# Optimization experiments

Measured on AMD Instinct MI355X. Metric: run time of the kernel, lower is better.

## Reference

```python
import jax, jax.numpy as jnp
import numpy as np

V = 33279   # num_tokens
E = 256     # embedding_size
H = 512     # hidden_size
NH = 8      # num_heads
L = 4       # num_layers
DH = E // NH
MAXPOS = 64


def _ln(x, g, b):
    mu = jnp.mean(x, axis=-1, keepdims=True)
    var = jnp.mean((x - mu) ** 2, axis=-1, keepdims=True)
    return (x - mu) / jnp.sqrt(var + 1e-5) * g + b


def setup_inputs() -> dict:
    key = jax.random.key(0)
    ks = jax.random.split(key, 32)
    N, S = 128, 64
    label = jax.random.randint(ks[0], (N, S), 0, V)
    # Bernoulli(0.15) BERT-style mask (deterministic stand-in for torch sampling)
    mask = (jax.random.uniform(ks[1], (N, S)) < 0.15).astype(jnp.int32)
    s = 0.02
    inp = {
        'label': label, 'mask': mask,
        'emb': jax.random.normal(ks[2], (V + 1, E)) * s,
        'pos': jax.random.normal(ks[3], (MAXPOS, E)) * s,
        'emb_g': jnp.ones((E,)), 'emb_b': jnp.zeros((E,)),
        # stacked per-layer params (leading dim L)
        'Wq': jax.random.normal(ks[4], (L, E, E)) * s, 'bq': jnp.zeros((L, E)),
        'Wk': jax.random.normal(ks[5], (L, E, E)) * s, 'bk': jnp.zeros((L, E)),
        'Wv': jax.random.normal(ks[6], (L, E, E)) * s, 'bv': jnp.zeros((L, E)),
        'Wo': jax.random.normal(ks[7], (L, E, E)) * s, 'bo': jnp.zeros((L, E)),
        'n1g': jnp.ones((L, E)), 'n1b': jnp.zeros((L, E)),
        'W1': jax.random.normal(ks[8], (L, E, H)) * s, 'b1': jnp.zeros((L, H)),
        'W2': jax.random.normal(ks[9], (L, H, E)) * s, 'b2': jnp.zeros((L, E)),
        'n2g': jnp.ones((L, E)), 'n2b': jnp.zeros((L, E)),
        # decoder head
        'dW1': jax.random.normal(ks[10], (E, E)) * s, 'db1': jnp.zeros((E,)),
        'dng': jnp.ones((E,)), 'dnb': jnp.zeros((E,)),
        'dW2': jax.random.normal(ks[11], (E, V)) * s, 'db2': jnp.zeros((V,)),
    }
    return inp


def reference(label, mask, emb, pos, emb_g, emb_b, Wq, bq, Wk, bk, Wv, bv,
              Wo, bo, n1g, n1b, W1, b1, W2, b2, n2g, n2b,
              dW1, db1, dng, dnb, dW2, db2):
    N, S = label.shape
    src_ids = jnp.where(mask == 1, V, label)  # masked-token id = num_tokens
    # embedding + positional, then LayerNorm (eval: Scaler/Dropout identity)
    x = emb[src_ids] + pos[:S][None, :, :]
    x = _ln(x, emb_g, emb_b)
    temp = jnp.asarray((E // NH) ** 0.5, x.dtype)

    def layer(x, p):
        wq, bq_, wk, bk_, wv, bv_, wo, bo_, g1, b1n, w1, b1_, w2, b2_, g2, b2n = p
        q = (x @ wq + bq_).reshape(N, S, NH, DH).transpose(0, 2, 1, 3)
        k = (x @ wk + bk_).reshape(N, S, NH, DH).transpose(0, 2, 1, 3)
        v = (x @ wv + bv_).reshape(N, S, NH, DH).transpose(0, 2, 1, 3)
        scores = jnp.einsum('nhsd,nhtd->nhst', q, k) / temp
        attn = jax.nn.softmax(scores, axis=-1)
        o = jnp.einsum('nhst,nhtd->nhsd', attn, v)
        o = o.transpose(0, 2, 1, 3).reshape(N, S, E) @ wo + bo_
        x1 = _ln(x + o, g1, b1n)
        ff = jax.nn.gelu(x1 @ w1 + b1_, approximate=False) @ w2 + b2_
        x2 = _ln(x1 + ff, g2, b2n)
        return x2, None

    x, _ = jax.lax.scan(layer, x, (Wq, bq, Wk, bk, Wv, bv, Wo, bo,
                                   n1g, n1b, W1, b1, W2, b2, n2g, n2b))
    # decoder head: linear -> gelu -> LN -> vocab projection
    h = jax.nn.gelu(x @ dW1 + db1, approximate=False)
    h = _ln(h, dng, dnb)
    logits = h @ dW2 + db2               # [N, S, V]
    logp = jax.nn.log_softmax(logits, axis=-1)
    loss = -jnp.take_along_axis(logp, label[..., None], axis=-1).mean()
    score = logits.transpose(0, 2, 1)    # [N, V, S] like torch permute(0,2,1)
    return score, loss
```

## Files before the change

### kernel.cpp

```cpp
#include <hip/hip_runtime.h>
#include <hip/hip_bf16.h>

#define DEVFN static __device__ __forceinline__

constexpr int N_ = 128, S_ = 64, T_ = N_ * S_;
constexpr int E_ = 256, H_ = 512, NH_ = 8, DH_ = 32, L_ = 4;
constexpr int V_ = 33279, VPAD_ = 33280, NVT_ = VPAD_ / 256;

typedef __attribute__((ext_vector_type(8))) short bf16x8;
typedef __attribute__((ext_vector_type(4))) float f32x4;
typedef unsigned short ushort_t;

DEVFN ushort_t f2bf(float f) {
  unsigned int u = __float_as_uint(f);
  unsigned int r = (u + 0x7fffu + ((u >> 16) & 1u)) >> 16;
  return (ushort_t)r;
}
DEVFN float bf2f(ushort_t u) { return __uint_as_float(((unsigned)u) << 16); }

DEVFN float geluf(float x) {
  return 0.5f * x * (1.f + erff(x * 0.70710678118654752440f));
}

DEVFN float wave_sum(float v) {
  #pragma unroll
  for (int off = 32; off >= 1; off >>= 1) v += __shfl_xor(v, off, 64);
  return v;
}

__global__ __launch_bounds__(256) void k_embed_ln(
    const int* __restrict__ label, const int* __restrict__ mask,
    const float* __restrict__ emb, const float* __restrict__ pos,
    const float* __restrict__ g, const float* __restrict__ b,
    float* __restrict__ x, ushort_t* __restrict__ xb) {
  int wv = threadIdx.x >> 6, lane = threadIdx.x & 63;
  int t = blockIdx.x * 4 + wv;
  int s = t & (S_ - 1);
  int id = (mask[t] == 1) ? V_ : label[t];
  int c = lane * 4;
  float4 v = *(const float4*)&emb[(size_t)id * E_ + c];
  float4 p = *(const float4*)&pos[s * E_ + c];
  v.x += p.x; v.y += p.y; v.z += p.z; v.w += p.w;
  float mean = wave_sum(v.x + v.y + v.z + v.w) * (1.f / E_);
  float4 d = {v.x - mean, v.y - mean, v.z - mean, v.w - mean};
  float var = wave_sum(d.x * d.x + d.y * d.y + d.z * d.z + d.w * d.w) * (1.f / E_);
  float rstd = 1.f / sqrtf(var + 1e-5f);
  float4 g4 = *(const float4*)&g[c];
  float4 b4 = *(const float4*)&b[c];
  float4 y = {d.x * rstd * g4.x + b4.x, d.y * rstd * g4.y + b4.y,
              d.z * rstd * g4.z + b4.z, d.w * rstd * g4.w + b4.w};
  *(float4*)&x[(size_t)t * E_ + c] = y;
  ushort4 yb = {f2bf(y.x), f2bf(y.y), f2bf(y.z), f2bf(y.w)};
  *(ushort4*)&xb[(size_t)t * E_ + c] = yb;
}

__global__ __launch_bounds__(256) void k_add_ln(
    const float* __restrict__ a, const float* __restrict__ bsrc,
    const float* __restrict__ g, const float* __restrict__ bet,
    float* __restrict__ y, ushort_t* __restrict__ yb) {
  int wv = threadIdx.x >> 6, lane = threadIdx.x & 63;
  int t = blockIdx.x * 4 + wv;
  int c = lane * 4;
  float4 v = *(const float4*)&a[(size_t)t * E_ + c];
  if (bsrc) {
    float4 u = *(const float4*)&bsrc[(size_t)t * E_ + c];
    v.x += u.x; v.y += u.y; v.z += u.z; v.w += u.w;
  }
  float mean = wave_sum(v.x + v.y + v.z + v.w) * (1.f / E_);
  float4 d = {v.x - mean, v.y - mean, v.z - mean, v.w - mean};
  float var = wave_sum(d.x * d.x + d.y * d.y + d.z * d.z + d.w * d.w) * (1.f / E_);
  float rstd = 1.f / sqrtf(var + 1e-5f);
  float4 g4 = *(const float4*)&g[c];
  float4 b4 = *(const float4*)&bet[c];
  float4 o = {d.x * rstd * g4.x + b4.x, d.y * rstd * g4.y + b4.y,
              d.z * rstd * g4.z + b4.z, d.w * rstd * g4.w + b4.w};
  if (y) *(float4*)&y[(size_t)t * E_ + c] = o;
  if (yb) {
    ushort4 ob = {f2bf(o.x), f2bf(o.y), f2bf(o.z), f2bf(o.w)};
    *(ushort4*)&yb[(size_t)t * E_ + c] = ob;
  }
}

__global__ __launch_bounds__(256) void k_bcat(
    const float* __restrict__ bq, const float* __restrict__ bk,
    const float* __restrict__ bv, float* __restrict__ bqkv) {
  int l = blockIdx.x, i = threadIdx.x;
  bqkv[l * 768 + i]       = bq[l * 256 + i];
  bqkv[l * 768 + 256 + i] = bk[l * 256 + i];
  bqkv[l * 768 + 512 + i] = bv[l * 256 + i];
}

__global__ __launch_bounds__(256) void k_wt(const float* __restrict__ src,
                                            ushort_t* __restrict__ dst,
                                            int K, int J, int dstLayerStride) {
  __shared__ float tile[32][33];
  int j0 = blockIdx.x * 32, k0 = blockIdx.y * 32, l = blockIdx.z;
  src += (size_t)l * K * J;
  dst += (size_t)l * dstLayerStride;
  int tx = threadIdx.x & 31, ty = threadIdx.x >> 5;
  #pragma unroll
  for (int rr = 0; rr < 4; rr++) {
    int kk = ty * 4 + rr;
    tile[kk][tx] = src[(size_t)(k0 + kk) * J + j0 + tx];
  }
  __syncthreads();
  #pragma unroll
  for (int rr = 0; rr < 4; rr++) {
    int jj = ty * 4 + rr;
    dst[(size_t)(j0 + jj) * K + k0 + tx] = f2bf(tile[tx][jj]);
  }
}

__global__ __launch_bounds__(256) void k_wtE(
    const float* __restrict__ Wq, const float* __restrict__ Wk,
    const float* __restrict__ Wv, const float* __restrict__ Wo,
    const float* __restrict__ dW1, ushort_t* __restrict__ wqkvT,
    ushort_t* __restrict__ woT, ushort_t* __restrict__ dw1T) {
  __shared__ float tile[32][33];
  int z = blockIdx.z;
  const float* src;
  ushort_t* dst;
  if (z == 4 * L_) {
    src = dW1; dst = dw1T;
  } else {
    int w = z >> 2, l = z & 3;
    const float* ws = (w == 0) ? Wq : (w == 1) ? Wk : (w == 2) ? Wv : Wo;
    src = ws + (size_t)l * E_ * E_;
    dst = (w < 3) ? (wqkvT + (size_t)l * 768 * E_ + (size_t)w * 256 * E_)
                  : (woT + (size_t)l * E_ * E_);
  }
  int j0 = blockIdx.x * 32, k0 = blockIdx.y * 32;
  int tx = threadIdx.x & 31, ty = threadIdx.x >> 5;
  #pragma unroll
  for (int rr = 0; rr < 4; rr++) {
    int kk = ty * 4 + rr;
    tile[kk][tx] = src[(size_t)(k0 + kk) * E_ + j0 + tx];
  }
  __syncthreads();
  #pragma unroll
  for (int rr = 0; rr < 4; rr++) {
    int jj = ty * 4 + rr;
    dst[(size_t)(j0 + jj) * E_ + k0 + tx] = f2bf(tile[tx][jj]);
  }
}

template <int K, int OUT_BF16, int GELU_>
__global__ __launch_bounds__(256) void k_mm(
    const ushort_t* __restrict__ Xb, const ushort_t* __restrict__ WT,
    const float* __restrict__ bias, void* __restrict__ C, int Nout) {
  constexpr int STR = K + 8;
  __shared__ ushort_t xs[64 * STR];
  int tid = threadIdx.x, lane = tid & 63, wv = tid >> 6;
  int t0 = blockIdx.x * 64, j0 = blockIdx.y * 64;
  const ushort_t* xsrc = Xb + (size_t)t0 * K;
  for (int i = tid; i < 64 * (K / 8); i += 256) {
    int r = i / (K / 8), c = (i % (K / 8)) * 8;
    *(uint4*)&xs[r * STR + c] = *(const uint4*)&xsrc[(size_t)r * K + c];
  }
  __syncthreads();
  int l15 = lane & 15, l4 = lane >> 4;
  f32x4 acc[4] = {};
  const ushort_t* xrow = &xs[(wv * 16 + l15) * STR + l4 * 8];
  const ushort_t* wrow = WT + (size_t)j0 * K + l4 * 8;
  #pragma unroll
  for (int kb = 0; kb < K / 32; kb++) {
    bf16x8 a = *(const bf16x8*)(xrow + kb * 32);
    #pragma unroll
    for (int st = 0; st < 4; st++) {
      bf16x8 bfr = *(const bf16x8*)(wrow + (size_t)(st * 16 + l15) * K + kb * 32);
      acc[st] = __builtin_amdgcn_mfma_f32_16x16x32_bf16(a, bfr, acc[st], 0, 0, 0);
    }
  }
  #pragma unroll
  for (int st = 0; st < 4; st++) {
    int j = j0 + st * 16 + l15;
    float bv_ = bias[j];
    #pragma unroll
    for (int r = 0; r < 4; r++) {
      float val = acc[st][r] + bv_;
      if (GELU_) val = geluf(val);
      int t = t0 + wv * 16 + l4 * 4 + r;
      if (OUT_BF16)
        ((ushort_t*)C)[(size_t)t * Nout + j] = f2bf(val);
      else
        ((float*)C)[(size_t)t * Nout + j] = val;
    }
  }
}

__global__ __launch_bounds__(256) void k_attn(
    const ushort_t* __restrict__ qkv, ushort_t* __restrict__ o) {
  __shared__ __align__(16) ushort_t vt_[32 * 72];
  __shared__ __align__(16) ushort_t ps[64 * 72];
  int n = blockIdx.x >> 3, h = blockIdx.x & 7;
  int tid = threadIdx.x, lane = tid & 63, wv = tid >> 6;
  int l15 = lane & 15, l4 = lane >> 4;
  const ushort_t* qbase = qkv + (size_t)n * S_ * 768 + h * DH_;
  for (int i = tid; i < S_ * DH_; i += 256) {
    int t = i >> 5, d = i & 31;
    vt_[d * 72 + t] = qbase[(size_t)t * 768 + 512 + d];
  }
  int srow = wv * 16 + l15;
  bf16x8 aq = *(const bf16x8*)&qbase[(size_t)srow * 768 + l4 * 8];
  f32x4 sc[4];
  #pragma unroll
  for (int st = 0; st < 4; st++) {
    bf16x8 bk_ = *(const bf16x8*)&qbase[(size_t)(st * 16 + l15) * 768 + 256 + l4 * 8];
    f32x4 z = {};
    sc[st] = __builtin_amdgcn_mfma_f32_16x16x32_bf16(aq, bk_, z, 0, 0, 0);
  }
  const float scale = 0.17677669529663687f;
  #pragma unroll
  for (int st = 0; st < 4; st++)
    #pragma unroll
    for (int r = 0; r < 4; r++) sc[st][r] *= scale;
  #pragma unroll
  for (int r = 0; r < 4; r++) {
    float m = fmaxf(fmaxf(sc[0][r], sc[1][r]), fmaxf(sc[2][r], sc[3][r]));
    m = fmaxf(m, __shfl_xor(m, 1, 64));
    m = fmaxf(m, __shfl_xor(m, 2, 64));
    m = fmaxf(m, __shfl_xor(m, 4, 64));
    m = fmaxf(m, __shfl_xor(m, 8, 64));
    float p0 = __expf(sc[0][r] - m), p1 = __expf(sc[1][r] - m);
    float p2 = __expf(sc[2][r] - m), p3 = __expf(sc[3][r] - m);
    float sum = p0 + p1 + p2 + p3;
    sum += __shfl_xor(sum, 1, 64);
    sum += __shfl_xor(sum, 2, 64);
    sum += __shfl_xor(sum, 4, 64);
    sum += __shfl_xor(sum, 8, 64);
    float inv = 1.f / sum;
    int prow = (wv * 16 + l4 * 4 + r) * 72;
    ps[prow + 0 * 16 + l15] = f2bf(p0 * inv);
    ps[prow + 1 * 16 + l15] = f2bf(p1 * inv);
    ps[prow + 2 * 16 + l15] = f2bf(p2 * inv);
    ps[prow + 3 * 16 + l15] = f2bf(p3 * inv);
  }
  __syncthreads();
  f32x4 oc[2] = {};
  #pragma unroll
  for (int kb = 0; kb < 2; kb++) {
    bf16x8 ap = *(const bf16x8*)&ps[srow * 72 + kb * 32 + l4 * 8];
    #pragma unroll
    for (int st2 = 0; st2 < 2; st2++) {
      bf16x8 bv_ = *(const bf16x8*)&vt_[(st2 * 16 + l15) * 72 + kb * 32 + l4 * 8];
      oc[st2] = __builtin_amdgcn_mfma_f32_16x16x32_bf16(ap, bv_, oc[st2], 0, 0, 0);
    }
  }
  ushort_t* ob = o + (size_t)n * S_ * E_ + h * DH_;
  #pragma unroll
  for (int st2 = 0; st2 < 2; st2++)
    #pragma unroll
    for (int r = 0; r < 4; r++)
      ob[(size_t)(wv * 16 + l4 * 4 + r) * E_ + st2 * 16 + l15] = f2bf(oc[st2][r]);
}

__global__ __launch_bounds__(256) void k_w2t(const float* __restrict__ w,
                                             ushort_t* __restrict__ wt) {
  __shared__ float tile[32 * 33];
  int tx = threadIdx.x & 31, ty = threadIdx.x >> 5;
  int v0 = blockIdx.x * 32, k0 = blockIdx.y * 32;
  #pragma unroll
  for (int rr = 0; rr < 4; rr++) {
    int kk = ty * 4 + rr;
    int vv = v0 + tx;
    tile[kk * 33 + tx] = (vv < V_) ? w[(size_t)(k0 + kk) * V_ + vv] : 0.f;
  }
  __syncthreads();
  #pragma unroll
  for (int rr = 0; rr < 4; rr++) {
    int vv = ty * 4 + rr;
    wt[(size_t)(v0 + vv) * E_ + k0 + tx] = f2bf(tile[tx * 33 + vv]);
  }
}

__global__ __launch_bounds__(256) void k_vocab(
    const ushort_t* __restrict__ hbf, const ushort_t* __restrict__ wt,
    const float* __restrict__ db2, float* __restrict__ out,
    float* __restrict__ pmax, float* __restrict__ psum) {
  __shared__ ushort_t hs[64 * 264];
  __shared__ float redm[4][64];
  __shared__ float reds[4][64];
  int n = blockIdx.x, vt = blockIdx.y;
  int tid = threadIdx.x, lane = tid & 63, wv = tid >> 6;
  const ushort_t* hsrc = hbf + (size_t)n * S_ * E_;
  for (int i = tid; i < (S_ * E_) / 8; i += 256) {
    int s = i >> 5, kc = (i & 31) * 8;
    *(uint4*)&hs[s * 264 + kc] = *(const uint4*)&hsrc[s * E_ + kc];
  }
  __syncthreads();
  int l15 = lane & 15, l4 = lane >> 4;
  float rm[4], rs[4];
  #pragma unroll
  for (int st = 0; st < 4; st++) { rm[st] = -INFINITY; rs[st] = 0.f; }
  #pragma unroll
  for (int h2 = 0; h2 < 2; h2++) {
    const ushort_t* Ap0 =
        wt + (size_t)(vt * 256 + h2 * 128 + wv * 16 + l15) * E_ + l4 * 8;
    const ushort_t* Ap1 = Ap0 + (size_t)64 * E_;
    f32x4 acc[2][4] = {};
    #pragma unroll
    for (int kb = 0; kb < 8; kb++) {
      bf16x8 a0 = *(const bf16x8*)(Ap0 + kb * 32);
      bf16x8 a1 = *(const bf16x8*)(Ap1 + kb * 32);
      #pragma unroll
      for (int st = 0; st < 4; st++) {
        bf16x8 bfr = *(const bf16x8*)&hs[(st * 16 + l15) * 264 + kb * 32 + l4 * 8];
        acc[0][st] = __builtin_amdgcn_mfma_f32_16x16x32_bf16(a0, bfr, acc[0][st], 0, 0, 0);
        acc[1][st] = __builtin_amdgcn_mfma_f32_16x16x32_bf16(a1, bfr, acc[1][st], 0, 0, 0);
      }
    }
    float vals[2][4][4];
    #pragma unroll
    for (int mt = 0; mt < 2; mt++) {
      #pragma unroll
      for (int j = 0; j < 4; j++) {
        int v = vt * 256 + h2 * 128 + wv * 16 + mt * 64 + l4 * 4 + j;
        bool valid = v < V_;
        float bias = valid ? db2[v] : 0.f;
        size_t ob = ((size_t)n * V_ + v) * S_;
        #pragma unroll
        for (int st = 0; st < 4; st++) {
          float val = valid ? (acc[mt][st][j] + bias) : -INFINITY;
          vals[mt][st][j] = val;
          if (valid) __builtin_nontemporal_store(val, &out[ob + st * 16 + l15]);
        }
      }
    }
    #pragma unroll
    for (int st = 0; st < 4; st++) {
      float m = -INFINITY;
      #pragma unroll
      for (int mt = 0; mt < 2; mt++)
        #pragma unroll
        for (int j = 0; j < 4; j++) m = fmaxf(m, vals[mt][st][j]);
      m = fmaxf(m, __shfl_xor(m, 16, 64));
      m = fmaxf(m, __shfl_xor(m, 32, 64));
      float sum = 0.f;
      #pragma unroll
      for (int mt = 0; mt < 2; mt++)
        #pragma unroll
        for (int j = 0; j < 4; j++) sum += __expf(vals[mt][st][j] - m);
      sum += __shfl_xor(sum, 16, 64);
      sum += __shfl_xor(sum, 32, 64);
      float nm = fmaxf(rm[st], m);
      rs[st] = rs[st] * __expf(rm[st] - nm) + sum * __expf(m - nm);
      rm[st] = nm;
    }
  }
  if (l4 == 0) {
    #pragma unroll
    for (int st = 0; st < 4; st++) {
      redm[wv][st * 16 + l15] = rm[st];
      reds[wv][st * 16 + l15] = rs[st];
    }
  }
  __syncthreads();
  if (wv == 0 && l4 == 0) {
    #pragma unroll
    for (int st = 0; st < 4; st++) {
      int s = st * 16 + l15;
      float M = fmaxf(fmaxf(redm[0][s], redm[1][s]), fmaxf(redm[2][s], redm[3][s]));
      float Sa = reds[0][s] * __expf(redm[0][s] - M) +
                 reds[1][s] * __expf(redm[1][s] - M) +
                 reds[2][s] * __expf(redm[2][s] - M) +
                 reds[3][s] * __expf(redm[3][s] - M);
      size_t pi = ((size_t)n * NVT_ + vt) * S_ + s;
      pmax[pi] = M;
      psum[pi] = Sa;
    }
  }
}

__global__ __launch_bounds__(512) void k_lossf(
    const float* __restrict__ pmax, const float* __restrict__ psum,
    const float* __restrict__ out, const int* __restrict__ label,
    float* __restrict__ partial) {
  __shared__ float sm[512], ssum[512];
  int n = blockIdx.x, tid = threadIdx.x;
  int s = tid & 63, qq = tid >> 6;
  float m = -INFINITY, sum = 0.f;
  for (int vt = qq; vt < NVT_; vt += 8) {
    size_t pi = ((size_t)n * NVT_ + vt) * S_ + s;
    float m2 = pmax[pi], s2 = psum[pi];
    float nm = fmaxf(m, m2);
    sum = sum * __expf(m - nm) + s2 * __expf(m2 - nm);
    m = nm;
  }
  sm[tid] = m; ssum[tid] = sum;
  __syncthreads();
  if (qq == 0) {
    float M = sm[s], Sa = ssum[s];
    #pragma unroll
    for (int p = 1; p < 8; p++) {
      float m2 = sm[p * 64 + s], s2 = ssum[p * 64 + s];
      float nm = fmaxf(M, m2);
      Sa = Sa * __expf(M - nm) + s2 * __expf(m2 - nm);
      M = nm;
    }
    float lse = M + logf(Sa);
    int lab = label[n * S_ + s];
    float lx = out[((size_t)n * V_ + lab) * S_ + s];
    partial[n * S_ + s] = lse - lx;
  }
}

__global__ __launch_bounds__(256) void k_loss2(const float* __restrict__ partial,
                                               float* __restrict__ dst) {
  __shared__ float sbuf[4];
  int tid = threadIdx.x;
  float acc = 0.f;
  for (int i = tid; i < T_; i += 256) acc += partial[i];
  #pragma unroll
  for (int off = 32; off >= 1; off >>= 1) acc += __shfl_xor(acc, off, 64);
  int lane = tid & 63, wid = tid >> 6;
  if (lane == 0) sbuf[wid] = acc;
  __syncthreads();
  if (tid == 0) dst[0] = (sbuf[0] + sbuf[1] + sbuf[2] + sbuf[3]) / (float)T_;
}

extern "C" void kernel_launch(void* const* d_in, const int* in_sizes, int n_in,
                              void* d_out, int out_size, void* d_ws, size_t ws_size,
                              hipStream_t stream) {
  const int*   label = (const int*)d_in[0];
  const int*   mask  = (const int*)d_in[1];
  const float* emb   = (const float*)d_in[2];
  const float* pos   = (const float*)d_in[3];
  const float* emb_g = (const float*)d_in[4];
  const float* emb_b = (const float*)d_in[5];
  const float* Wq  = (const float*)d_in[6];
  const float* bq  = (const float*)d_in[7];
  const float* Wk  = (const float*)d_in[8];
  const float* bk  = (const float*)d_in[9];
  const float* Wv  = (const float*)d_in[10];
  const float* bv  = (const float*)d_in[11];
  const float* Wo  = (const float*)d_in[12];
  const float* bo  = (const float*)d_in[13];
  const float* n1g = (const float*)d_in[14];
  const float* n1b = (const float*)d_in[15];
  const float* W1  = (const float*)d_in[16];
  const float* b1  = (const float*)d_in[17];
  const float* W2  = (const float*)d_in[18];
  const float* b2  = (const float*)d_in[19];
  const float* n2g = (const float*)d_in[20];
  const float* n2b = (const float*)d_in[21];
  const float* dW1 = (const float*)d_in[22];
  const float* db1 = (const float*)d_in[23];
  const float* dng = (const float*)d_in[24];
  const float* dnb = (const float*)d_in[25];
  const float* dW2 = (const float*)d_in[26];
  const float* db2 = (const float*)d_in[27];
  float* out = (float*)d_out;
  (void)in_sizes; (void)n_in; (void)out_size; (void)ws_size;

  char* base = (char*)d_ws;
  size_t off = 0;
  auto alloc = [&](size_t bytes) {
    char* p = base + off;
    off += (bytes + 255) & ~(size_t)255;
    return p;
  };
  float*    x    = (float*)alloc((size_t)T_ * E_ * 4);
  ushort_t* xb   = (ushort_t*)alloc((size_t)T_ * E_ * 2);
  float*    x1   = (float*)alloc((size_t)T_ * E_ * 4);
  ushort_t* x1b  = (ushort_t*)alloc((size_t)T_ * E_ * 2);
  ushort_t* qkv  = (ushort_t*)alloc((size_t)T_ * 768 * 2);
  ushort_t* obuf = (ushort_t*)alloc((size_t)T_ * E_ * 2);
  float*    ftmp = (float*)alloc((size_t)T_ * E_ * 4);
  ushort_t* wqkvT = (ushort_t*)alloc((size_t)L_ * 768 * E_ * 2);
  ushort_t* woT   = (ushort_t*)alloc((size_t)L_ * E_ * E_ * 2);
  ushort_t* w1T   = (ushort_t*)alloc((size_t)L_ * H_ * E_ * 2);
  ushort_t* w2T   = (ushort_t*)alloc((size_t)L_ * E_ * H_ * 2);
  ushort_t* dw1T  = (ushort_t*)alloc((size_t)E_ * E_ * 2);
  ushort_t* wt    = (ushort_t*)alloc((size_t)VPAD_ * E_ * 2);
  float*    bqkv  = (float*)alloc((size_t)L_ * 768 * 4);
  float*    partial = (float*)alloc((size_t)T_ * 4);
  ushort_t* ffh = qkv;
  ushort_t* hbf = obuf;
  float* pmax = x;
  float* psum = pmax + (size_t)N_ * NVT_ * S_;

  k_bcat<<<L_, 256, 0, stream>>>(bq, bk, bv, bqkv);
  k_wtE<<<dim3(8, 8, 4 * L_ + 1), 256, 0, stream>>>(Wq, Wk, Wv, Wo, dW1, wqkvT, woT, dw1T);
  k_wt<<<dim3(16, 8, L_), 256, 0, stream>>>(W1, w1T, E_, H_, H_ * E_);
  k_wt<<<dim3(8, 16, L_), 256, 0, stream>>>(W2, w2T, H_, E_, E_ * H_);
  k_w2t<<<dim3(VPAD_ / 32, E_ / 32), 256, 0, stream>>>(dW2, wt);

  k_embed_ln<<<T_ / 4, 256, 0, stream>>>(label, mask, emb, pos, emb_g, emb_b, x, xb);

  for (int l = 0; l < L_; l++) {
    k_mm<E_, 1, 0><<<dim3(T_ / 64, 12), 256, 0, stream>>>(
        xb, wqkvT + (size_t)l * 768 * E_, bqkv + l * 768, qkv, 768);
    k_attn<<<N_ * NH_, 256, 0, stream>>>(qkv, obuf);
    k_mm<E_, 0, 0><<<dim3(T_ / 64, 4), 256, 0, stream>>>(
        obuf, woT + (size_t)l * E_ * E_, bo + l * E_, ftmp, E_);
    k_add_ln<<<T_ / 4, 256, 0, stream>>>(x, ftmp, n1g + l * E_, n1b + l * E_, x1, x1b);
    k_mm<E_, 1, 1><<<dim3(T_ / 64, 8), 256, 0, stream>>>(
        x1b, w1T + (size_t)l * H_ * E_, b1 + l * H_, ffh, H_);
    k_mm<H_, 0, 0><<<dim3(T_ / 64, 4), 256, 0, stream>>>(
        ffh, w2T + (size_t)l * E_ * H_, b2 + l * E_, ftmp, E_);
    k_add_ln<<<T_ / 4, 256, 0, stream>>>(x1, ftmp, n2g + l * E_, n2b + l * E_, x, xb);
  }

  k_mm<E_, 0, 1><<<dim3(T_ / 64, 4), 256, 0, stream>>>(xb, dw1T, db1, ftmp, E_);
  k_add_ln<<<T_ / 4, 256, 0, stream>>>(ftmp, nullptr, dng, dnb, nullptr, hbf);

  k_vocab<<<dim3(N_, NVT_), 256, 0, stream>>>(hbf, wt, db2, out, pmax, psum);

  k_lossf<<<N_, 512, 0, stream>>>(pmax, psum, out, label, partial);
  k_loss2<<<1, 256, 0, stream>>>(partial, out + (size_t)N_ * V_ * S_);
}
```

Measured before the change: 923.0 us.

## Fuse output projections with residual add and LayerNorm into one kernel

Adds a k_mm_ln2 kernel in which each block computes 16 full token rows of a K→256 GEMM, then adds bias, residual (or GELU) and applies LayerNorm in-register using cross-wave reductions through shared memory. It replaces the separate matmul plus k_add_ln pairs for the attention output, the FFN down projection and the decoder first linear, removing the fp32 ftmp round-trip and several launches. The trade-off is smaller 16-row tiles in which every block rereads the whole weight matrix from global/L2 memory, so weight reuse per block drops.

```diff
diff --git a/kernel.cpp b/kernel.cpp
--- a/kernel.cpp
+++ b/kernel.cpp
@@ -25,6 +25,14 @@
 DEVFN float wave_sum(float v) {
   #pragma unroll
   for (int off = 32; off >= 1; off >>= 1) v += __shfl_xor(v, off, 64);
+  return v;
+}
+
+DEVFN float l15_sum(float v) {
+  v += __shfl_xor(v, 1, 64);
+  v += __shfl_xor(v, 2, 64);
+  v += __shfl_xor(v, 4, 64);
+  v += __shfl_xor(v, 8, 64);
   return v;
 }
 
@@ -54,33 +62,6 @@
   *(ushort4*)&xb[(size_t)t * E_ + c] = yb;
 }
 
-__global__ __launch_bounds__(256) void k_add_ln(
-    const float* __restrict__ a, const float* __restrict__ bsrc,
-    const float* __restrict__ g, const float* __restrict__ bet,
-    float* __restrict__ y, ushort_t* __restrict__ yb) {
-  int wv = threadIdx.x >> 6, lane = threadIdx.x & 63;
-  int t = blockIdx.x * 4 + wv;
-  int c = lane * 4;
-  float4 v = *(const float4*)&a[(size_t)t * E_ + c];
-  if (bsrc) {
-    float4 u = *(const float4*)&bsrc[(size_t)t * E_ + c];
-    v.x += u.x; v.y += u.y; v.z += u.z; v.w += u.w;
-  }
-  float mean = wave_sum(v.x + v.y + v.z + v.w) * (1.f / E_);
-  float4 d = {v.x - mean, v.y - mean, v.z - mean, v.w - mean};
-  float var = wave_sum(d.x * d.x + d.y * d.y + d.z * d.z + d.w * d.w) * (1.f / E_);
-  float rstd = 1.f / sqrtf(var + 1e-5f);
-  float4 g4 = *(const float4*)&g[c];
-  float4 b4 = *(const float4*)&bet[c];
-  float4 o = {d.x * rstd * g4.x + b4.x, d.y * rstd * g4.y + b4.y,
-              d.z * rstd * g4.z + b4.z, d.w * rstd * g4.w + b4.w};
-  if (y) *(float4*)&y[(size_t)t * E_ + c] = o;
-  if (yb) {
-    ushort4 ob = {f2bf(o.x), f2bf(o.y), f2bf(o.z), f2bf(o.w)};
-    *(ushort4*)&yb[(size_t)t * E_ + c] = ob;
-  }
-}
-
 __global__ __launch_bounds__(256) void k_bcat(
     const float* __restrict__ bq, const float* __restrict__ bk,
     const float* __restrict__ bv, float* __restrict__ bqkv) {
@@ -184,6 +165,95 @@
         ((ushort_t*)C)[(size_t)t * Nout + j] = f2bf(val);
       else
         ((float*)C)[(size_t)t * Nout + j] = val;
+    }
+  }
+}
+
+template <int K, int GELU_PRE, int HAS_RES, int OUT_F32>
+__global__ __launch_bounds__(256) void k_mm_ln2(
+    const ushort_t* __restrict__ Xb, const ushort_t* __restrict__ WT,
+    const float* __restrict__ bias, const float* __restrict__ res,
+    const float* __restrict__ g, const float* __restrict__ bet,
+    float* __restrict__ y, ushort_t* __restrict__ yb) {
+  constexpr int STR = K + 8;
+  __shared__ ushort_t xs[16 * STR];
+  __shared__ float redA[4][16], redB[4][16];
+  int tid = threadIdx.x, lane = tid & 63, wv = tid >> 6;
+  int t0 = blockIdx.x * 16;
+  const ushort_t* xsrc = Xb + (size_t)t0 * K;
+  for (int i = tid; i < 16 * (K / 8); i += 256) {
+    int r = i / (K / 8), c = (i % (K / 8)) * 8;
+    *(uint4*)&xs[r * STR + c] = *(const uint4*)&xsrc[(size_t)r * K + c];
+  }
+  __syncthreads();
+  int l15 = lane & 15, l4 = lane >> 4;
+  f32x4 acc[4] = {};
+  const ushort_t* xrow = &xs[l15 * STR + l4 * 8];
+  const ushort_t* wrow = WT + (size_t)(wv * 64) * K + l4 * 8;
+  #pragma unroll
+  for (int kb = 0; kb < K / 32; kb++) {
+    bf16x8 a = *(const bf16x8*)(xrow + kb * 32);
+    #pragma unroll
+    for (int st = 0; st < 4; st++) {
+      bf16x8 bfr = *(const bf16x8*)(wrow + (size_t)(st * 16 + l15) * K + kb * 32);
+      acc[st] = __builtin_amdgcn_mfma_f32_16x16x32_bf16(a, bfr, acc[st], 0, 0, 0);
+    }
+  }
+  float val[4][4];
+  #pragma unroll
+  for (int st = 0; st < 4; st++) {
+    int j = wv * 64 + st * 16 + l15;
+    float bv_ = bias[j];
+    #pragma unroll
+    for (int r = 0; r < 4; r++) {
+      float v = acc[st][r] + bv_;
+      if (GELU_PRE) v = geluf(v);
+      if (HAS_RES) v += res[(size_t)(t0 + l4 * 4 + r) * E_ + j];
+      val[st][r] = v;
+    }
+  }
+  #pragma unroll
+  for (int r = 0; r < 4; r++) {
+    float s = val[0][r] + val[1][r] + val[2][r] + val[3][r];
+    s = l15_sum(s);
+    if (l15 == 0) redA[wv][l4 * 4 + r] = s;
+  }
+  __syncthreads();
+  float mean[4];
+  #pragma unroll
+  for (int r = 0; r < 4; r++) {
+    int row = l4 * 4 + r;
+    mean[r] = (redA[0][row] + redA[1][row] + redA[2][row] + redA[3][row]) * (1.f / E_);
+  }
+  #pragma unroll
+  for (int r = 0; r < 4; r++) {
+    float s = 0.f;
+    #pragma unroll
+    for (int st = 0; st < 4; st++) {
+      float d = val[st][r] - mean[r];
+      s += d * d;
+    }
+    s = l15_sum(s);
+    if (l15 == 0) redB[wv][l4 * 4 + r] = s;
+  }
+  __syncthreads();
+  float rstd[4];
+  #pragma unroll
+  for (int r = 0; r < 4; r++) {
+    int row = l4 * 4 + r;
+    float var = (redB[0][row] + redB[1][row] + redB[2][row] + redB[3][row]) * (1.f / E_);
+    rstd[r] = 1.f / sqrtf(var + 1e-5f);
+  }
+  #pragma unroll
+  for (int st = 0; st < 4; st++) {
+    int j = wv * 64 + st * 16 + l15;
+    float gj = g[j], bj = bet[j];
+    #pragma unroll
+    for (int r = 0; r < 4; r++) {
+      int t = t0 + l4 * 4 + r;
+      float o = (val[st][r] - mean[r]) * rstd[r] * gj + bj;
+      if (OUT_F32) y[(size_t)t * E_ + j] = o;
+      yb[(size_t)t * E_ + j] = f2bf(o);
     }
   }
 }
@@ -465,7 +535,6 @@
   ushort_t* x1b  = (ushort_t*)alloc((size_t)T_ * E_ * 2);
   ushort_t* qkv  = (ushort_t*)alloc((size_t)T_ * 768 * 2);
   ushort_t* obuf = (ushort_t*)alloc((size_t)T_ * E_ * 2);
-  float*    ftmp = (float*)alloc((size_t)T_ * E_ * 4);
   ushort_t* wqkvT = (ushort_t*)alloc((size_t)L_ * 768 * E_ * 2);
   ushort_t* woT   = (ushort_t*)alloc((size_t)L_ * E_ * E_ * 2);
   ushort_t* w1T   = (ushort_t*)alloc((size_t)L_ * H_ * E_ * 2);
@@ -491,18 +560,18 @@
     k_mm<E_, 1, 0><<<dim3(T_ / 64, 12), 256, 0, stream>>>(
         xb, wqkvT + (size_t)l * 768 * E_, bqkv + l * 768, qkv, 768);
     k_attn<<<N_ * NH_, 256, 0, stream>>>(qkv, obuf);
-    k_mm<E_, 0, 0><<<dim3(T_ / 64, 4), 256, 0, stream>>>(
-        obuf, woT + (size_t)l * E_ * E_, bo + l * E_, ftmp, E_);
-    k_add_ln<<<T_ / 4, 256, 0, stream>>>(x, ftmp, n1g + l * E_, n1b + l * E_, x1, x1b);
+    k_mm_ln2<E_, 0, 1, 1><<<T_ / 16, 256, 0, stream>>>(
+        obuf, woT + (size_t)l * E_ * E_, bo + l * E_, x,
+        n1g + l * E_, n1b + l * E_, x1, x1b);
     k_mm<E_, 1, 1><<<dim3(T_ / 64, 8), 256, 0, stream>>>(
         x1b, w1T + (size_t)l * H_ * E_, b1 + l * H_, ffh, H_);
-    k_mm<H_, 0, 0><<<dim3(T_ / 64, 4), 256, 0, stream>>>(
-        ffh, w2T + (size_t)l * E_ * H_, b2 + l * E_, ftmp, E_);
-    k_add_ln<<<T_ / 4, 256, 0, stream>>>(x1, ftmp, n2g + l * E_, n2b + l * E_, x, xb);
-  }
-
-  k_mm<E_, 0, 1><<<dim3(T_ / 64, 4), 256, 0, stream>>>(xb, dw1T, db1, ftmp, E_);
-  k_add_ln<<<T_ / 4, 256, 0, stream>>>(ftmp, nullptr, dng, dnb, nullptr, hbf);
+    k_mm_ln2<H_, 0, 1, 1><<<T_ / 16, 256, 0, stream>>>(
+        ffh, w2T + (size_t)l * E_ * H_, b2 + l * E_, x1,
+        n2g + l * E_, n2b + l * E_, x, xb);
+  }
+
+  k_mm_ln2<E_, 1, 0, 0><<<T_ / 16, 256, 0, stream>>>(
+      xb, dw1T, db1, nullptr, dng, dnb, nullptr, hbf);
 
   k_vocab<<<dim3(N_, NVT_), 256, 0, stream>>>(hbf, wt, db2, out, pmax, psum);
 
```

Result: faster. 875.6 us (-5.1%).
